# Kernel optimization log

Measured on AMD Instinct MI355X. Metric: run time of the kernel, lower is better.

Reference implementation:

```python
import jax, jax.numpy as jnp
import numpy as np
import math

HIDDEN = 1024
HEADS = 16
HEAD_DIM = HIDDEN // HEADS
TEMP_K = 1000.0  # custom temperature multiplier applied after masking
B, S = 2, 2048


def setup_inputs() -> dict:
    key = jax.random.key(0)
    ks = jax.random.split(key, 4)
    scale = 1.0 / math.sqrt(HIDDEN)
    return {
        "x": jax.random.normal(ks[0], (B, S, HIDDEN), dtype=jnp.float32),
        "W_qkv": jax.random.normal(ks[1], (HIDDEN, 3 * HIDDEN), dtype=jnp.float32) * scale,
        "b_qkv": jnp.zeros((3 * HIDDEN,), dtype=jnp.float32),
        "W_out": jax.random.normal(ks[2], (HIDDEN, HIDDEN), dtype=jnp.float32) * scale,
        "b_out": jnp.zeros((HIDDEN,), dtype=jnp.float32),
    }


def reference(x, W_qkv, b_qkv, W_out, b_out):
    b, s, _ = x.shape
    qkv = x @ W_qkv + b_qkv                                    # [b,s,3*hidden]
    qkv = qkv.reshape(b, s, 3, HEADS, HEAD_DIM)
    qkv = jnp.transpose(qkv, (2, 0, 3, 1, 4))                  # [3,b,h,s,d]
    q, k, v = qkv[0], qkv[1], qkv[2]
    scores = jnp.einsum('bhqd,bhkd->bhqk', q, k) / math.sqrt(HEAD_DIM)
    causal = jnp.tril(jnp.ones((s, s), dtype=bool))            # [s,s]
    scores = jnp.where(causal[None, None], scores, -jnp.inf)
    probs = jax.nn.softmax(scores * TEMP_K, axis=-1)           # temp-scaled softmax
    attn = jnp.einsum('bhqk,bhkd->bhqd', probs, v)             # [b,h,s,d]
    attn = jnp.transpose(attn, (0, 2, 1, 3)).reshape(b, s, HIDDEN)
    return attn @ W_out + b_out
```

## Files before the change

### kernel.cpp

```cpp
#include <hip/hip_runtime.h>
#include <hip/hip_bf16.h>

#define BATCH 2
#define SEQ 2048
#define HID 1024
#define NHEAD 16
#define HDIM 64
#define L2SCALE 180.3368800721f
#define NEGBIG (-1.0e30f)
#define N_ITEMS 512

typedef __bf16 bf16;
typedef __bf16 bf16x4 __attribute__((ext_vector_type(4)));
typedef __bf16 bf16x8 __attribute__((ext_vector_type(8)));
typedef float f32x16 __attribute__((ext_vector_type(16)));

union BQ  { bf16x4 v; unsigned u[2]; };
union BF8 { bf16x8 v; unsigned u[4]; };

__global__ __launch_bounds__(256) void transpose_split_kernel(
    const float* __restrict__ W, bf16* __restrict__ Thi, bf16* __restrict__ Tlo,
    int K, int N)
{
    __shared__ float T[64][65];
    const int tid = threadIdx.x;
    const int kBase = blockIdx.y * 64;
    const int nBase = blockIdx.x * 64;
    {
        const int k0 = tid >> 4;
        const int nc = (tid & 15) * 4;
#pragma unroll
        for (int kk = 0; kk < 4; kk++) {
            int k = k0 + kk * 16;
            float4 v = *(const float4*)(W + (size_t)(kBase + k) * N + nBase + nc);
            T[k][nc] = v.x; T[k][nc + 1] = v.y; T[k][nc + 2] = v.z; T[k][nc + 3] = v.w;
        }
    }
    __syncthreads();
    {
        const int n = tid >> 2;
        const int kc = (tid & 3) * 16;
        bf16x8 h0, h1, l0, l1;
#pragma unroll
        for (int j = 0; j < 8; j++) {
            float a = T[kc + j][n];
            float c = T[kc + 8 + j][n];
            bf16 ha = (bf16)a, hc = (bf16)c;
            h0[j] = ha; h1[j] = hc;
            l0[j] = (bf16)(a - (float)ha);
            l1[j] = (bf16)(c - (float)hc);
        }
        size_t dst = (size_t)(nBase + n) * K + kBase + kc;
        *(bf16x8*)(Thi + dst)     = h0;
        *(bf16x8*)(Thi + dst + 8) = h1;
        if (Tlo) {
            *(bf16x8*)(Tlo + dst)     = l0;
            *(bf16x8*)(Tlo + dst + 8) = l1;
        }
    }
}

__global__ __launch_bounds__(256) void xsplit_kernel(
    const float* __restrict__ X, bf16* __restrict__ Xhi, bf16* __restrict__ Xlo,
    unsigned* __restrict__ ctr)
{
    if (blockIdx.x == 0 && threadIdx.x == 0) *ctr = 0u;
    const int i = blockIdx.x * 256 + threadIdx.x;
    float4 v = ((const float4*)X)[i];
    float xs[4] = {v.x, v.y, v.z, v.w};
    bf16x4 h, l;
#pragma unroll
    for (int j = 0; j < 4; j++) {
        h[j] = (bf16)xs[j];
        l[j] = (bf16)(xs[j] - (float)h[j]);
    }
    ((bf16x4*)Xhi)[i] = h;
    ((bf16x4*)Xlo)[i] = l;
}

__global__ __launch_bounds__(256) void vtrans_kernel(
    const bf16* __restrict__ vv, bf16* __restrict__ vtr)
{
    __shared__ bf16 T[64][72];
    const int tid = threadIdx.x;
    const int bh = blockIdx.y;
    const int st = blockIdx.x;
    const int r  = tid >> 2;
    const int c0 = (tid & 3) * 16;
    const bf16* src = vv + ((size_t)bh * SEQ + st * 64) * HDIM;
    bf16x8 a = *(const bf16x8*)(src + (size_t)r * HDIM + c0);
    bf16x8 b = *(const bf16x8*)(src + (size_t)r * HDIM + c0 + 8);
    *(bf16x8*)&T[r][c0]     = a;
    *(bf16x8*)&T[r][c0 + 8] = b;
    __syncthreads();
    bf16x8 o0, o1;
#pragma unroll
    for (int i = 0; i < 8; i++) {
        o0[i] = T[c0 + i][r];
        o1[i] = T[c0 + 8 + i][r];
    }
    bf16* dst = vtr + ((size_t)bh * HDIM + r) * SEQ + st * 64 + c0;
    *(bf16x8*)(dst)     = o0;
    *(bf16x8*)(dst + 8) = o1;
}

__global__ __launch_bounds__(256) void gemm_qkv_mfma(
    const bf16* __restrict__ Xhi, const bf16* __restrict__ Xlo,
    const bf16* __restrict__ Wthi, const bf16* __restrict__ Wtlo,
    const float* __restrict__ bias,
    bf16* __restrict__ qhi, bf16* __restrict__ qlo,
    bf16* __restrict__ khi, bf16* __restrict__ klo, bf16* __restrict__ vv)
{
    __shared__ __align__(16) bf16 Xh[128][40];
    __shared__ __align__(16) bf16 Xl[128][40];
    __shared__ __align__(16) bf16 Wh[128][40];
    __shared__ __align__(16) bf16 Wl[128][40];

    const int tid = threadIdx.x;
    const int wave = tid >> 6, lane = tid & 63;
    const int lm = lane & 31, lq2 = lane >> 5;
    const int wave_s = wave & 1, wave_n = wave >> 1;
    const int nBase = blockIdx.x * 128;
    const int sBase = blockIdx.y * 128;
    const bool isV = (nBase >= 2 * HID);

    const int sr = tid >> 1, skc = (tid & 1) * 16;

    f32x16 acc[2][2];
#pragma unroll
    for (int st = 0; st < 2; st++)
#pragma unroll
      for (int nt = 0; nt < 2; nt++)
#pragma unroll
        for (int r = 0; r < 16; r++) acc[st][nt][r] = 0.f;

    bf16x8 cx[2], cw[2], cxl[2] = {}, cwl[2] = {};
    {
        size_t xsrc = (size_t)(sBase + sr) * HID + skc;
        size_t wsrc = (size_t)(nBase + sr) * HID + skc;
        cx[0] = *(const bf16x8*)(Xhi + xsrc);
        cx[1] = *(const bf16x8*)(Xhi + xsrc + 8);
        cw[0] = *(const bf16x8*)(Wthi + wsrc);
        cw[1] = *(const bf16x8*)(Wthi + wsrc + 8);
        if (!isV) {
            cxl[0] = *(const bf16x8*)(Xlo + xsrc);
            cxl[1] = *(const bf16x8*)(Xlo + xsrc + 8);
            cwl[0] = *(const bf16x8*)(Wtlo + wsrc);
            cwl[1] = *(const bf16x8*)(Wtlo + wsrc + 8);
        }
    }

    for (int k0 = 0; k0 < HID; k0 += 32) {
        __syncthreads();
        *(bf16x8*)&Xh[sr][skc]     = cx[0];
        *(bf16x8*)&Xh[sr][skc + 8] = cx[1];
        *(bf16x8*)&Wh[sr][skc]     = cw[0];
        *(bf16x8*)&Wh[sr][skc + 8] = cw[1];
        if (!isV) {
            *(bf16x8*)&Xl[sr][skc]     = cxl[0];
            *(bf16x8*)&Xl[sr][skc + 8] = cxl[1];
            *(bf16x8*)&Wl[sr][skc]     = cwl[0];
            *(bf16x8*)&Wl[sr][skc + 8] = cwl[1];
        }
        __syncthreads();

        bf16x8 nx[2] = {}, nw[2] = {}, nxl[2] = {}, nwl[2] = {};
        if (k0 + 32 < HID) {
            size_t xsrc = (size_t)(sBase + sr) * HID + k0 + 32 + skc;
            size_t wsrc = (size_t)(nBase + sr) * HID + k0 + 32 + skc;
            nx[0] = *(const bf16x8*)(Xhi + xsrc);
            nx[1] = *(const bf16x8*)(Xhi + xsrc + 8);
            nw[0] = *(const bf16x8*)(Wthi + wsrc);
            nw[1] = *(const bf16x8*)(Wthi + wsrc + 8);
            if (!isV) {
                nxl[0] = *(const bf16x8*)(Xlo + xsrc);
                nxl[1] = *(const bf16x8*)(Xlo + xsrc + 8);
                nwl[0] = *(const bf16x8*)(Wtlo + wsrc);
                nwl[1] = *(const bf16x8*)(Wtlo + wsrc + 8);
            }
        }

#pragma unroll
        for (int kh = 0; kh < 2; kh++) {
            const int ko = kh * 16 + lq2 * 8;
            bf16x8 aWh[2], aWl[2], bXh[2], bXl[2];
#pragma unroll
            for (int nt = 0; nt < 2; nt++) {
                aWh[nt] = *(bf16x8*)&Wh[wave_n * 64 + nt * 32 + lm][ko];
                if (!isV) aWl[nt] = *(bf16x8*)&Wl[wave_n * 64 + nt * 32 + lm][ko];
            }
#pragma unroll
            for (int st = 0; st < 2; st++) {
                bXh[st] = *(bf16x8*)&Xh[wave_s * 64 + st * 32 + lm][ko];
                if (!isV) bXl[st] = *(bf16x8*)&Xl[wave_s * 64 + st * 32 + lm][ko];
            }
#pragma unroll
            for (int nt = 0; nt < 2; nt++)
#pragma unroll
              for (int st = 0; st < 2; st++) {
                acc[st][nt] = __builtin_amdgcn_mfma_f32_32x32x16_bf16(aWh[nt], bXh[st], acc[st][nt], 0, 0, 0);
                if (!isV) {
                    acc[st][nt] = __builtin_amdgcn_mfma_f32_32x32x16_bf16(aWh[nt], bXl[st], acc[st][nt], 0, 0, 0);
                    acc[st][nt] = __builtin_amdgcn_mfma_f32_32x32x16_bf16(aWl[nt], bXh[st], acc[st][nt], 0, 0, 0);
                }
              }
        }
        cx[0] = nx[0]; cx[1] = nx[1]; cw[0] = nw[0]; cw[1] = nw[1];
        cxl[0] = nxl[0]; cxl[1] = nxl[1]; cwl[0] = nwl[0]; cwl[1] = nwl[1];
    }

#pragma unroll
    for (int st = 0; st < 2; st++) {
        int s = sBase + wave_s * 64 + st * 32 + lm;
        int bb = s >> 11, ss = s & 2047;
#pragma unroll
        for (int nt = 0; nt < 2; nt++) {
#pragma unroll
            for (int q4 = 0; q4 < 4; q4++) {
                int n = nBase + wave_n * 64 + nt * 32 + 8 * q4 + 4 * lq2;
                float4 bv = *(const float4*)(bias + n);
                float vals[4];
                vals[0] = acc[st][nt][q4 * 4 + 0] + bv.x;
                vals[1] = acc[st][nt][q4 * 4 + 1] + bv.y;
                vals[2] = acc[st][nt][q4 * 4 + 2] + bv.z;
                vals[3] = acc[st][nt][q4 * 4 + 3] + bv.w;
                int which = n >> 10, h = (n >> 6) & 15, d = n & 63;
                size_t dst = (((size_t)bb * NHEAD + h) * SEQ + ss) * HDIM + d;
                if (which < 2) {
                    bf16x4 hi4, lo4;
#pragma unroll
                    for (int i = 0; i < 4; i++) {
                        hi4[i] = (bf16)vals[i];
                        lo4[i] = (bf16)(vals[i] - (float)hi4[i]);
                    }
                    bf16* ph = (which == 0) ? qhi : khi;
                    bf16* pl = (which == 0) ? qlo : klo;
                    *(bf16x4*)(ph + dst) = hi4;
                    *(bf16x4*)(pl + dst) = lo4;
                } else {
                    bf16x4 v4;
#pragma unroll
                    for (int i = 0; i < 4; i++) v4[i] = (bf16)vals[i];
                    *(bf16x4*)(vv + dst) = v4;
                }
            }
        }
    }
}

__global__ __launch_bounds__(256) void attn_kernel(
    const bf16* __restrict__ Qhi, const bf16* __restrict__ Qlo,
    const bf16* __restrict__ Khg, const bf16* __restrict__ Klg,
    const bf16* __restrict__ Vtr, bf16* __restrict__ attnbuf,
    unsigned* __restrict__ ctr)
{
    __shared__ __align__(16) bf16 Khs[64][72];
    __shared__ __align__(16) bf16 Kls[64][72];
    __shared__ __align__(16) bf16 Vt [64][72];
    __shared__ int s_item;

    const int tid  = threadIdx.x;
    const int wave = tid >> 6;
    const int lane = tid & 63;
    const int lm   = lane & 31;
    const int lq2  = lane >> 5;

    const int kr  = tid >> 2;
    const int kd0 = (tid & 3) * 16;

    for (;;) {
        if (tid == 0) s_item = (int)atomicAdd(ctr, 1u);
        __syncthreads();
        const int it = s_item;
        if (it >= N_ITEMS) return;
        const int qt = 15 - (it >> 5);
        const int bh = it & 31;
        const int b = bh >> 4, h = bh & 15;
        const size_t headoff = ((size_t)b * NHEAD + h) * SEQ * HDIM;

        const int qg = qt * 128 + wave * 32 + lm;
        bf16x8 qh[4], ql[4];
        {
            const bf16* qph = Qhi + headoff + (size_t)qg * HDIM;
            const bf16* qpl = Qlo + headoff + (size_t)qg * HDIM;
#pragma unroll
            for (int c = 0; c < 4; c++) {
                qh[c] = *(const bf16x8*)(qph + c * 16 + lq2 * 8);
                ql[c] = *(const bf16x8*)(qpl + c * 16 + lq2 * 8);
            }
        }

        f32x16 O0, O1;
#pragma unroll
        for (int r = 0; r < 16; r++) { O0[r] = 0.f; O1[r] = 0.f; }
        float m_run = NEGBIG, l_run = 0.f;

        const int ktmax = 2 * qt + 1;
        bf16x8 kc[4], vc[2];
        {
            size_t kg = headoff + (size_t)kr * HDIM + kd0;
            kc[0] = *(const bf16x8*)(Khg + kg);
            kc[1] = *(const bf16x8*)(Khg + kg + 8);
            kc[2] = *(const bf16x8*)(Klg + kg);
            kc[3] = *(const bf16x8*)(Klg + kg + 8);
            size_t vg = headoff + (size_t)kr * SEQ + kd0;
            vc[0] = *(const bf16x8*)(Vtr + vg);
            vc[1] = *(const bf16x8*)(Vtr + vg + 8);
        }

        for (int kt = 0; kt <= ktmax; kt++) {
            __syncthreads();
            *(bf16x8*)&Khs[kr][kd0]     = kc[0];
            *(bf16x8*)&Khs[kr][kd0 + 8] = kc[1];
            *(bf16x8*)&Kls[kr][kd0]     = kc[2];
            *(bf16x8*)&Kls[kr][kd0 + 8] = kc[3];
            *(bf16x8*)&Vt[kr][kd0]      = vc[0];
            *(bf16x8*)&Vt[kr][kd0 + 8]  = vc[1];
            __syncthreads();

            bf16x8 kn[4], vn[2];
            const bool more = (kt < ktmax);
            if (more) {
                size_t kg = headoff + (size_t)((kt + 1) * 64 + kr) * HDIM + kd0;
                kn[0] = *(const bf16x8*)(Khg + kg);
                kn[1] = *(const bf16x8*)(Khg + kg + 8);
                kn[2] = *(const bf16x8*)(Klg + kg);
                kn[3] = *(const bf16x8*)(Klg + kg + 8);
                size_t vg = headoff + (size_t)kr * SEQ + (kt + 1) * 64 + kd0;
                vn[0] = *(const bf16x8*)(Vtr + vg);
                vn[1] = *(const bf16x8*)(Vtr + vg + 8);
            }

            if (kt * 64 <= qt * 128 + wave * 32 + 31) {
                f32x16 s[2];
#pragma unroll
                for (int r = 0; r < 16; r++) { s[0][r] = 0.f; s[1][r] = 0.f; }
#pragma unroll
                for (int c = 0; c < 4; c++) {
                    bf16x8 ah0 = *(bf16x8*)&Khs[lm][c * 16 + lq2 * 8];
                    bf16x8 al0 = *(bf16x8*)&Kls[lm][c * 16 + lq2 * 8];
                    bf16x8 ah1 = *(bf16x8*)&Khs[32 + lm][c * 16 + lq2 * 8];
                    bf16x8 al1 = *(bf16x8*)&Kls[32 + lm][c * 16 + lq2 * 8];
                    s[0] = __builtin_amdgcn_mfma_f32_32x32x16_bf16(ah0, qh[c], s[0], 0, 0, 0);
                    s[0] = __builtin_amdgcn_mfma_f32_32x32x16_bf16(ah0, ql[c], s[0], 0, 0, 0);
                    s[0] = __builtin_amdgcn_mfma_f32_32x32x16_bf16(al0, qh[c], s[0], 0, 0, 0);
                    s[1] = __builtin_amdgcn_mfma_f32_32x32x16_bf16(ah1, qh[c], s[1], 0, 0, 0);
                    s[1] = __builtin_amdgcn_mfma_f32_32x32x16_bf16(ah1, ql[c], s[1], 0, 0, 0);
                    s[1] = __builtin_amdgcn_mfma_f32_32x32x16_bf16(al1, qh[c], s[1], 0, 0, 0);
                }

                const int kbase = kt * 64 + 4 * lq2;
                const bool needmask = (kt * 64 + 63 > qg);
#pragma unroll
                for (int mt = 0; mt < 2; mt++)
#pragma unroll
                  for (int r = 0; r < 16; r++) {
                    int koff = (r & 3) + 8 * (r >> 2) + 32 * mt;
                    float L = s[mt][r] * L2SCALE;
                    if (needmask && (kbase + koff > qg)) L = NEGBIG;
                    s[mt][r] = L;
                  }

                float vmax = NEGBIG;
#pragma unroll
                for (int r = 0; r < 16; r++)
                    vmax = fmaxf(vmax, fmaxf(s[0][r], s[1][r]));
                vmax = fmaxf(vmax, __shfl_xor(vmax, 32, 64));
                float mnew = fmaxf(m_run, vmax);
                float alpha = exp2f(m_run - mnew);
                float sum = 0.f;
#pragma unroll
                for (int mt = 0; mt < 2; mt++)
#pragma unroll
                  for (int r = 0; r < 16; r++) {
                    s[mt][r] = exp2f(s[mt][r] - mnew);
                    sum += s[mt][r];
                  }
                sum += __shfl_xor(sum, 32, 64);
                l_run = l_run * alpha + sum;
                m_run = mnew;
#pragma unroll
                for (int r = 0; r < 16; r++) { O0[r] *= alpha; O1[r] *= alpha; }

                bf16x8 pfrag[4];
#pragma unroll
                for (int mt = 0; mt < 2; mt++)
#pragma unroll
                  for (int hh = 0; hh < 2; hh++) {
                    BQ A, B;
#pragma unroll
                    for (int i = 0; i < 4; i++) {
                        A.v[i] = (bf16)s[mt][8 * hh + i];
                        B.v[i] = (bf16)s[mt][8 * hh + 4 + i];
                    }
                    unsigned s0_ = lq2 ? A.u[0] : B.u[0];
                    unsigned s1_ = lq2 ? A.u[1] : B.u[1];
                    unsigned r0 = __shfl_xor(s0_, 32, 64);
                    unsigned r1 = __shfl_xor(s1_, 32, 64);
                    BF8 f;
                    f.u[0] = lq2 ? r0 : A.u[0];
                    f.u[1] = lq2 ? r1 : A.u[1];
                    f.u[2] = lq2 ? B.u[0] : r0;
                    f.u[3] = lq2 ? B.u[1] : r1;
                    pfrag[mt * 2 + hh] = f.v;
                  }

#pragma unroll
                for (int c = 0; c < 4; c++) {
                    bf16x8 va0 = *(bf16x8*)&Vt[lm][c * 16 + lq2 * 8];
                    bf16x8 va1 = *(bf16x8*)&Vt[32 + lm][c * 16 + lq2 * 8];
                    O0 = __builtin_amdgcn_mfma_f32_32x32x16_bf16(va0, pfrag[c], O0, 0, 0, 0);
                    O1 = __builtin_amdgcn_mfma_f32_32x32x16_bf16(va1, pfrag[c], O1, 0, 0, 0);
                }
            }

            if (more) {
#pragma unroll
                for (int i = 0; i < 4; i++) kc[i] = kn[i];
                vc[0] = vn[0]; vc[1] = vn[1];
            }
        }

        const float inv = 1.0f / l_run;
        bf16* orow = attnbuf + ((size_t)b * SEQ + qg) * HID + h * HDIM;
#pragma unroll
        for (int g = 0; g < 4; g++) {
            int d0 = 8 * g + 4 * lq2;
            bf16x4 o0, o1;
#pragma unroll
            for (int i = 0; i < 4; i++) {
                o0[i] = (bf16)(O0[4 * g + i] * inv);
                o1[i] = (bf16)(O1[4 * g + i] * inv);
            }
            *(bf16x4*)(orow + d0)      = o0;
            *(bf16x4*)(orow + 32 + d0) = o1;
        }
    }
}

__global__ __launch_bounds__(256) void gemm_out_mfma(
    const bf16* __restrict__ Attn, const bf16* __restrict__ Wt,
    const float* __restrict__ bias, float* __restrict__ out)
{
    __shared__ __align__(16) bf16 Ah[64][40];
    __shared__ __align__(16) bf16 Bh[128][40];

    const int tid = threadIdx.x;
    const int wave = tid >> 6, lane = tid & 63;
    const int lm = lane & 31, lq2 = lane >> 5;
    const int nBase = blockIdx.x * 64;
    const int mBase = blockIdx.y * 128;

    const int sr = tid >> 1, skc = (tid & 1) * 16;
    const int ar = tid >> 2, akc = (tid & 3) * 8;

    f32x16 acc[2];
#pragma unroll
    for (int nt = 0; nt < 2; nt++)
#pragma unroll
      for (int r = 0; r < 16; r++) acc[nt][r] = 0.f;

    bf16x8 cb[2], ca;
    {
        cb[0] = *(const bf16x8*)(Attn + (size_t)(mBase + sr) * HID + skc);
        cb[1] = *(const bf16x8*)(Attn + (size_t)(mBase + sr) * HID + skc + 8);
        ca    = *(const bf16x8*)(Wt + (size_t)(nBase + ar) * HID + akc);
    }

    for (int k0 = 0; k0 < HID; k0 += 32) {
        __syncthreads();
        *(bf16x8*)&Bh[sr][skc]     = cb[0];
        *(bf16x8*)&Bh[sr][skc + 8] = cb[1];
        *(bf16x8*)&Ah[ar][akc]     = ca;
        __syncthreads();

        bf16x8 nb[2] = {}, na = {};
        if (k0 + 32 < HID) {
            nb[0] = *(const bf16x8*)(Attn + (size_t)(mBase + sr) * HID + k0 + 32 + skc);
            nb[1] = *(const bf16x8*)(Attn + (size_t)(mBase + sr) * HID + k0 + 32 + skc + 8);
            na    = *(const bf16x8*)(Wt + (size_t)(nBase + ar) * HID + k0 + 32 + akc);
        }
#pragma unroll
        for (int kh = 0; kh < 2; kh++) {
            const int ko = kh * 16 + lq2 * 8;
            bf16x8 bA  = *(bf16x8*)&Bh[wave * 32 + lm][ko];
            bf16x8 aW0 = *(bf16x8*)&Ah[lm][ko];
            bf16x8 aW1 = *(bf16x8*)&Ah[32 + lm][ko];
            acc[0] = __builtin_amdgcn_mfma_f32_32x32x16_bf16(aW0, bA, acc[0], 0, 0, 0);
            acc[1] = __builtin_amdgcn_mfma_f32_32x32x16_bf16(aW1, bA, acc[1], 0, 0, 0);
        }
        cb[0] = nb[0]; cb[1] = nb[1]; ca = na;
    }

    const int m = mBase + wave * 32 + lm;
#pragma unroll
    for (int nt = 0; nt < 2; nt++) {
#pragma unroll
        for (int q4 = 0; q4 < 4; q4++) {
            int n = nBase + nt * 32 + 8 * q4 + 4 * lq2;
            float4 bv = *(const float4*)(bias + n);
            float4 o;
            o.x = acc[nt][q4 * 4 + 0] + bv.x;
            o.y = acc[nt][q4 * 4 + 1] + bv.y;
            o.z = acc[nt][q4 * 4 + 2] + bv.z;
            o.w = acc[nt][q4 * 4 + 3] + bv.w;
            *(float4*)(out + (size_t)m * HID + n) = o;
        }
    }
}

extern "C" void kernel_launch(void* const* d_in, const int* in_sizes, int n_in,
                              void* d_out, int out_size, void* d_ws, size_t ws_size,
                              hipStream_t stream) {
    const float* x    = (const float*)d_in[0];
    const float* Wqkv = (const float*)d_in[1];
    const float* bqkv = (const float*)d_in[2];
    const float* Wout = (const float*)d_in[3];
    const float* bout = (const float*)d_in[4];
    float* out = (float*)d_out;

    const size_t NW  = (size_t)HID * 3 * HID;
    const size_t NWo = (size_t)HID * HID;
    const size_t NT  = (size_t)BATCH * NHEAD * SEQ * HDIM;
    bf16* Wthi = (bf16*)d_ws;
    bf16* Wtlo = Wthi + NW;
    bf16* Wot  = Wtlo + NW;
    bf16* qhi  = Wot + NWo;
    bf16* qlo  = qhi + NT;
    bf16* khi  = qlo + NT;
    bf16* klo  = khi + NT;
    bf16* vv   = klo + NT;
    bf16* attnbuf = vv + NT;
    bf16* Xhi  = attnbuf;
    bf16* Xlo  = attnbuf + NT;
    bf16* vtr  = Xlo;
    unsigned* ctr = (unsigned*)(Xlo + NT);

    xsplit_kernel<<<dim3((BATCH * SEQ * HID) / 1024), 256, 0, stream>>>(x, Xhi, Xlo, ctr);
    transpose_split_kernel<<<dim3(3 * HID / 64, HID / 64), 256, 0, stream>>>(
        Wqkv, Wthi, Wtlo, HID, 3 * HID);
    transpose_split_kernel<<<dim3(HID / 64, HID / 64), 256, 0, stream>>>(
        Wout, Wot, nullptr, HID, HID);
    gemm_qkv_mfma<<<dim3(3 * HID / 128, BATCH * SEQ / 128), 256, 0, stream>>>(
        Xhi, Xlo, Wthi, Wtlo, bqkv, qhi, qlo, khi, klo, vv);
    vtrans_kernel<<<dim3(SEQ / 64, BATCH * NHEAD), 256, 0, stream>>>(vv, vtr);
    attn_kernel<<<dim3(1024), 256, 0, stream>>>(
        qhi, qlo, khi, klo, vtr, attnbuf, ctr);
    gemm_out_mfma<<<dim3(HID / 64, BATCH * SEQ / 128), 256, 0, stream>>>(
        attnbuf, Wot, bout, out);
}
```

Before: 277.4 us.

## Replace atomic work queue with static split-KV schedule plus combine kernel

Drops the atomic-counter persistent scheduler for attention. A static table of 30 slots per head gives each block a balanced chunk of at most 12 key tiles, and long query tiles are split across 2–3 blocks. Partial outputs and their (m,l) statistics go to scratch buffers reused from dead workspace, and a new combine kernel merges them. Masking is also limited to the diagonal tiles. This evens out causal load across the 960 blocks, at the cost of an extra launch, partial-output traffic, and rounding the partials to bf16.

```diff
diff --git a/kernel.cpp b/kernel.cpp
--- a/kernel.cpp
+++ b/kernel.cpp
@@ -8,7 +8,6 @@
 #define HDIM 64
 #define L2SCALE 180.3368800721f
 #define NEGBIG (-1.0e30f)
-#define N_ITEMS 512
 
 typedef __bf16 bf16;
 typedef __bf16 bf16x4 __attribute__((ext_vector_type(4)));
@@ -17,6 +16,11 @@
 
 union BQ  { bf16x4 v; unsigned u[2]; };
 union BF8 { bf16x8 v; unsigned u[4]; };
+
+__device__ __constant__ int TAB_QT[30]  = {5,6,7,8,9,10,11,11,12,12,13,13,14,14,15,15, 4,10, 3,9,15, 2,8,14, 1,7,13, 0,6,12};
+__device__ __constant__ int TAB_K0[30]  = {0,0,0,0,0,0,0,12,0,12,0,12,0,12,0,12, 0,12, 0,12,24, 0,12,24, 0,12,24, 0,12,24};
+__device__ __constant__ int TAB_NIT[30] = {12,12,12,12,12,12,12,12,12,12,12,12,12,12,12,12, 10,10, 8,8,8, 6,6,6, 4,4,4, 2,2,2};
+__device__ __constant__ int TAB_PID[30] = {-1,0,2,4,6,8,10,11,12,13,15,16,18,19,21,22, -1,9, -1,7,23, -1,5,20, -1,3,17, -1,1,14};
 
 __global__ __launch_bounds__(256) void transpose_split_kernel(
     const float* __restrict__ W, bf16* __restrict__ Thi, bf16* __restrict__ Tlo,
@@ -61,10 +65,8 @@
 }
 
 __global__ __launch_bounds__(256) void xsplit_kernel(
-    const float* __restrict__ X, bf16* __restrict__ Xhi, bf16* __restrict__ Xlo,
-    unsigned* __restrict__ ctr)
+    const float* __restrict__ X, bf16* __restrict__ Xhi, bf16* __restrict__ Xlo)
 {
-    if (blockIdx.x == 0 && threadIdx.x == 0) *ctr = 0u;
     const int i = blockIdx.x * 256 + threadIdx.x;
     float4 v = ((const float4*)X)[i];
     float xs[4] = {v.x, v.y, v.z, v.w};
@@ -252,12 +254,11 @@
     const bf16* __restrict__ Qhi, const bf16* __restrict__ Qlo,
     const bf16* __restrict__ Khg, const bf16* __restrict__ Klg,
     const bf16* __restrict__ Vtr, bf16* __restrict__ attnbuf,
-    unsigned* __restrict__ ctr)
+    bf16* __restrict__ PartO, float* __restrict__ Mls)
 {
     __shared__ __align__(16) bf16 Khs[64][72];
     __shared__ __align__(16) bf16 Kls[64][72];
     __shared__ __align__(16) bf16 Vt [64][72];
-    __shared__ int s_item;
 
     const int tid  = threadIdx.x;
     const int wave = tid >> 6;
@@ -268,159 +269,168 @@
     const int kr  = tid >> 2;
     const int kd0 = (tid & 3) * 16;
 
-    for (;;) {
-        if (tid == 0) s_item = (int)atomicAdd(ctr, 1u);
+    const int slot = blockIdx.x >> 5;
+    const int bh   = blockIdx.x & 31;
+    const int qt   = TAB_QT[slot];
+    const int kt0  = TAB_K0[slot];
+    const int nit  = TAB_NIT[slot];
+    const int pid  = TAB_PID[slot];
+    const int b = bh >> 4, h = bh & 15;
+    const size_t headoff = ((size_t)b * NHEAD + h) * SEQ * HDIM;
+
+    const int ql_loc = wave * 32 + lm;
+    const int qg = qt * 128 + ql_loc;
+    bf16x8 qh[4], qlr[4];
+    {
+        const bf16* qph = Qhi + headoff + (size_t)qg * HDIM;
+        const bf16* qpl = Qlo + headoff + (size_t)qg * HDIM;
+#pragma unroll
+        for (int c = 0; c < 4; c++) {
+            qh[c]  = *(const bf16x8*)(qph + c * 16 + lq2 * 8);
+            qlr[c] = *(const bf16x8*)(qpl + c * 16 + lq2 * 8);
+        }
+    }
+
+    f32x16 O0, O1;
+#pragma unroll
+    for (int r = 0; r < 16; r++) { O0[r] = 0.f; O1[r] = 0.f; }
+    float m_run = NEGBIG, l_run = 0.f;
+
+    const int wave_qmin = qt * 128 + wave * 32;
+    const int ktend = kt0 + nit;
+
+    bf16x8 kc[4], vc[2];
+    {
+        size_t kg = headoff + (size_t)(kt0 * 64 + kr) * HDIM + kd0;
+        kc[0] = *(const bf16x8*)(Khg + kg);
+        kc[1] = *(const bf16x8*)(Khg + kg + 8);
+        kc[2] = *(const bf16x8*)(Klg + kg);
+        kc[3] = *(const bf16x8*)(Klg + kg + 8);
+        size_t vg = headoff + (size_t)kr * SEQ + kt0 * 64 + kd0;
+        vc[0] = *(const bf16x8*)(Vtr + vg);
+        vc[1] = *(const bf16x8*)(Vtr + vg + 8);
+    }
+
+    for (int kt = kt0; kt < ktend; kt++) {
         __syncthreads();
-        const int it = s_item;
-        if (it >= N_ITEMS) return;
-        const int qt = 15 - (it >> 5);
-        const int bh = it & 31;
-        const int b = bh >> 4, h = bh & 15;
-        const size_t headoff = ((size_t)b * NHEAD + h) * SEQ * HDIM;
-
-        const int qg = qt * 128 + wave * 32 + lm;
-        bf16x8 qh[4], ql[4];
-        {
-            const bf16* qph = Qhi + headoff + (size_t)qg * HDIM;
-            const bf16* qpl = Qlo + headoff + (size_t)qg * HDIM;
+        *(bf16x8*)&Khs[kr][kd0]     = kc[0];
+        *(bf16x8*)&Khs[kr][kd0 + 8] = kc[1];
+        *(bf16x8*)&Kls[kr][kd0]     = kc[2];
+        *(bf16x8*)&Kls[kr][kd0 + 8] = kc[3];
+        *(bf16x8*)&Vt[kr][kd0]      = vc[0];
+        *(bf16x8*)&Vt[kr][kd0 + 8]  = vc[1];
+        __syncthreads();
+
+        bf16x8 kn[4], vn[2];
+        const bool more = (kt + 1 < ktend);
+        if (more) {
+            size_t kg = headoff + (size_t)((kt + 1) * 64 + kr) * HDIM + kd0;
+            kn[0] = *(const bf16x8*)(Khg + kg);
+            kn[1] = *(const bf16x8*)(Khg + kg + 8);
+            kn[2] = *(const bf16x8*)(Klg + kg);
+            kn[3] = *(const bf16x8*)(Klg + kg + 8);
+            size_t vg = headoff + (size_t)kr * SEQ + (kt + 1) * 64 + kd0;
+            vn[0] = *(const bf16x8*)(Vtr + vg);
+            vn[1] = *(const bf16x8*)(Vtr + vg + 8);
+        }
+
+        if (kt * 64 <= wave_qmin + 31) {
+            f32x16 s[2];
+#pragma unroll
+            for (int r = 0; r < 16; r++) { s[0][r] = 0.f; s[1][r] = 0.f; }
 #pragma unroll
             for (int c = 0; c < 4; c++) {
-                qh[c] = *(const bf16x8*)(qph + c * 16 + lq2 * 8);
-                ql[c] = *(const bf16x8*)(qpl + c * 16 + lq2 * 8);
-            }
-        }
-
-        f32x16 O0, O1;
-#pragma unroll
-        for (int r = 0; r < 16; r++) { O0[r] = 0.f; O1[r] = 0.f; }
-        float m_run = NEGBIG, l_run = 0.f;
-
-        const int ktmax = 2 * qt + 1;
-        bf16x8 kc[4], vc[2];
-        {
-            size_t kg = headoff + (size_t)kr * HDIM + kd0;
-            kc[0] = *(const bf16x8*)(Khg + kg);
-            kc[1] = *(const bf16x8*)(Khg + kg + 8);
-            kc[2] = *(const bf16x8*)(Klg + kg);
-            kc[3] = *(const bf16x8*)(Klg + kg + 8);
-            size_t vg = headoff + (size_t)kr * SEQ + kd0;
-            vc[0] = *(const bf16x8*)(Vtr + vg);
-            vc[1] = *(const bf16x8*)(Vtr + vg + 8);
-        }
-
-        for (int kt = 0; kt <= ktmax; kt++) {
-            __syncthreads();
-            *(bf16x8*)&Khs[kr][kd0]     = kc[0];
-            *(bf16x8*)&Khs[kr][kd0 + 8] = kc[1];
-            *(bf16x8*)&Kls[kr][kd0]     = kc[2];
-            *(bf16x8*)&Kls[kr][kd0 + 8] = kc[3];
-            *(bf16x8*)&Vt[kr][kd0]      = vc[0];
-            *(bf16x8*)&Vt[kr][kd0 + 8]  = vc[1];
-            __syncthreads();
-
-            bf16x8 kn[4], vn[2];
-            const bool more = (kt < ktmax);
-            if (more) {
-                size_t kg = headoff + (size_t)((kt + 1) * 64 + kr) * HDIM + kd0;
-                kn[0] = *(const bf16x8*)(Khg + kg);
-                kn[1] = *(const bf16x8*)(Khg + kg + 8);
-                kn[2] = *(const bf16x8*)(Klg + kg);
-                kn[3] = *(const bf16x8*)(Klg + kg + 8);
-                size_t vg = headoff + (size_t)kr * SEQ + (kt + 1) * 64 + kd0;
-                vn[0] = *(const bf16x8*)(Vtr + vg);
-                vn[1] = *(const bf16x8*)(Vtr + vg + 8);
-            }
-
-            if (kt * 64 <= qt * 128 + wave * 32 + 31) {
-                f32x16 s[2];
-#pragma unroll
-                for (int r = 0; r < 16; r++) { s[0][r] = 0.f; s[1][r] = 0.f; }
-#pragma unroll
-                for (int c = 0; c < 4; c++) {
-                    bf16x8 ah0 = *(bf16x8*)&Khs[lm][c * 16 + lq2 * 8];
-                    bf16x8 al0 = *(bf16x8*)&Kls[lm][c * 16 + lq2 * 8];
-                    bf16x8 ah1 = *(bf16x8*)&Khs[32 + lm][c * 16 + lq2 * 8];
-                    bf16x8 al1 = *(bf16x8*)&Kls[32 + lm][c * 16 + lq2 * 8];
-                    s[0] = __builtin_amdgcn_mfma_f32_32x32x16_bf16(ah0, qh[c], s[0], 0, 0, 0);
-                    s[0] = __builtin_amdgcn_mfma_f32_32x32x16_bf16(ah0, ql[c], s[0], 0, 0, 0);
-                    s[0] = __builtin_amdgcn_mfma_f32_32x32x16_bf16(al0, qh[c], s[0], 0, 0, 0);
-                    s[1] = __builtin_amdgcn_mfma_f32_32x32x16_bf16(ah1, qh[c], s[1], 0, 0, 0);
-                    s[1] = __builtin_amdgcn_mfma_f32_32x32x16_bf16(ah1, ql[c], s[1], 0, 0, 0);
-                    s[1] = __builtin_amdgcn_mfma_f32_32x32x16_bf16(al1, qh[c], s[1], 0, 0, 0);
-                }
-
+                bf16x8 ah0 = *(bf16x8*)&Khs[lm][c * 16 + lq2 * 8];
+                bf16x8 al0 = *(bf16x8*)&Kls[lm][c * 16 + lq2 * 8];
+                bf16x8 ah1 = *(bf16x8*)&Khs[32 + lm][c * 16 + lq2 * 8];
+                bf16x8 al1 = *(bf16x8*)&Kls[32 + lm][c * 16 + lq2 * 8];
+                s[0] = __builtin_amdgcn_mfma_f32_32x32x16_bf16(ah0, qh[c],  s[0], 0, 0, 0);
+                s[0] = __builtin_amdgcn_mfma_f32_32x32x16_bf16(ah0, qlr[c], s[0], 0, 0, 0);
+                s[0] = __builtin_amdgcn_mfma_f32_32x32x16_bf16(al0, qh[c],  s[0], 0, 0, 0);
+                s[1] = __builtin_amdgcn_mfma_f32_32x32x16_bf16(ah1, qh[c],  s[1], 0, 0, 0);
+                s[1] = __builtin_amdgcn_mfma_f32_32x32x16_bf16(ah1, qlr[c], s[1], 0, 0, 0);
+                s[1] = __builtin_amdgcn_mfma_f32_32x32x16_bf16(al1, qh[c],  s[1], 0, 0, 0);
+            }
+
+            if (kt * 64 + 63 > wave_qmin) {
                 const int kbase = kt * 64 + 4 * lq2;
-                const bool needmask = (kt * 64 + 63 > qg);
 #pragma unroll
                 for (int mt = 0; mt < 2; mt++)
 #pragma unroll
                   for (int r = 0; r < 16; r++) {
                     int koff = (r & 3) + 8 * (r >> 2) + 32 * mt;
                     float L = s[mt][r] * L2SCALE;
-                    if (needmask && (kbase + koff > qg)) L = NEGBIG;
+                    if (kbase + koff > qg) L = NEGBIG;
                     s[mt][r] = L;
                   }
-
-                float vmax = NEGBIG;
-#pragma unroll
-                for (int r = 0; r < 16; r++)
-                    vmax = fmaxf(vmax, fmaxf(s[0][r], s[1][r]));
-                vmax = fmaxf(vmax, __shfl_xor(vmax, 32, 64));
-                float mnew = fmaxf(m_run, vmax);
-                float alpha = exp2f(m_run - mnew);
-                float sum = 0.f;
+            } else {
 #pragma unroll
                 for (int mt = 0; mt < 2; mt++)
 #pragma unroll
-                  for (int r = 0; r < 16; r++) {
-                    s[mt][r] = exp2f(s[mt][r] - mnew);
-                    sum += s[mt][r];
-                  }
-                sum += __shfl_xor(sum, 32, 64);
-                l_run = l_run * alpha + sum;
-                m_run = mnew;
-#pragma unroll
-                for (int r = 0; r < 16; r++) { O0[r] *= alpha; O1[r] *= alpha; }
-
-                bf16x8 pfrag[4];
-#pragma unroll
-                for (int mt = 0; mt < 2; mt++)
-#pragma unroll
-                  for (int hh = 0; hh < 2; hh++) {
-                    BQ A, B;
-#pragma unroll
-                    for (int i = 0; i < 4; i++) {
-                        A.v[i] = (bf16)s[mt][8 * hh + i];
-                        B.v[i] = (bf16)s[mt][8 * hh + 4 + i];
-                    }
-                    unsigned s0_ = lq2 ? A.u[0] : B.u[0];
-                    unsigned s1_ = lq2 ? A.u[1] : B.u[1];
-                    unsigned r0 = __shfl_xor(s0_, 32, 64);
-                    unsigned r1 = __shfl_xor(s1_, 32, 64);
-                    BF8 f;
-                    f.u[0] = lq2 ? r0 : A.u[0];
-                    f.u[1] = lq2 ? r1 : A.u[1];
-                    f.u[2] = lq2 ? B.u[0] : r0;
-                    f.u[3] = lq2 ? B.u[1] : r1;
-                    pfrag[mt * 2 + hh] = f.v;
-                  }
-
-#pragma unroll
-                for (int c = 0; c < 4; c++) {
-                    bf16x8 va0 = *(bf16x8*)&Vt[lm][c * 16 + lq2 * 8];
-                    bf16x8 va1 = *(bf16x8*)&Vt[32 + lm][c * 16 + lq2 * 8];
-                    O0 = __builtin_amdgcn_mfma_f32_32x32x16_bf16(va0, pfrag[c], O0, 0, 0, 0);
-                    O1 = __builtin_amdgcn_mfma_f32_32x32x16_bf16(va1, pfrag[c], O1, 0, 0, 0);
+                  for (int r = 0; r < 16; r++) s[mt][r] *= L2SCALE;
+            }
+
+            float vmax = NEGBIG;
+#pragma unroll
+            for (int r = 0; r < 16; r++)
+                vmax = fmaxf(vmax, fmaxf(s[0][r], s[1][r]));
+            vmax = fmaxf(vmax, __shfl_xor(vmax, 32, 64));
+            float mnew = fmaxf(m_run, vmax);
+            float alpha = exp2f(m_run - mnew);
+            float sum = 0.f;
+#pragma unroll
+            for (int mt = 0; mt < 2; mt++)
+#pragma unroll
+              for (int r = 0; r < 16; r++) {
+                s[mt][r] = exp2f(s[mt][r] - mnew);
+                sum += s[mt][r];
+              }
+            sum += __shfl_xor(sum, 32, 64);
+            l_run = l_run * alpha + sum;
+            m_run = mnew;
+#pragma unroll
+            for (int r = 0; r < 16; r++) { O0[r] *= alpha; O1[r] *= alpha; }
+
+            bf16x8 pfrag[4];
+#pragma unroll
+            for (int mt = 0; mt < 2; mt++)
+#pragma unroll
+              for (int hh = 0; hh < 2; hh++) {
+                BQ A, B;
+#pragma unroll
+                for (int i = 0; i < 4; i++) {
+                    A.v[i] = (bf16)s[mt][8 * hh + i];
+                    B.v[i] = (bf16)s[mt][8 * hh + 4 + i];
                 }
-            }
-
-            if (more) {
-#pragma unroll
-                for (int i = 0; i < 4; i++) kc[i] = kn[i];
-                vc[0] = vn[0]; vc[1] = vn[1];
-            }
-        }
-
+                unsigned s0_ = lq2 ? A.u[0] : B.u[0];
+                unsigned s1_ = lq2 ? A.u[1] : B.u[1];
+                unsigned r0 = __shfl_xor(s0_, 32, 64);
+                unsigned r1 = __shfl_xor(s1_, 32, 64);
+                BF8 f;
+                f.u[0] = lq2 ? r0 : A.u[0];
+                f.u[1] = lq2 ? r1 : A.u[1];
+                f.u[2] = lq2 ? B.u[0] : r0;
+                f.u[3] = lq2 ? B.u[1] : r1;
+                pfrag[mt * 2 + hh] = f.v;
+              }
+
+#pragma unroll
+            for (int c = 0; c < 4; c++) {
+                bf16x8 va0 = *(bf16x8*)&Vt[lm][c * 16 + lq2 * 8];
+                bf16x8 va1 = *(bf16x8*)&Vt[32 + lm][c * 16 + lq2 * 8];
+                O0 = __builtin_amdgcn_mfma_f32_32x32x16_bf16(va0, pfrag[c], O0, 0, 0, 0);
+                O1 = __builtin_amdgcn_mfma_f32_32x32x16_bf16(va1, pfrag[c], O1, 0, 0, 0);
+            }
+        }
+
+        if (more) {
+#pragma unroll
+            for (int i = 0; i < 4; i++) kc[i] = kn[i];
+            vc[0] = vn[0]; vc[1] = vn[1];
+        }
+    }
+
+    if (pid < 0) {
         const float inv = 1.0f / l_run;
         bf16* orow = attnbuf + ((size_t)b * SEQ + qg) * HID + h * HDIM;
 #pragma unroll
@@ -435,6 +445,78 @@
             *(bf16x4*)(orow + d0)      = o0;
             *(bf16x4*)(orow + 32 + d0) = o1;
         }
+    } else {
+        bf16* prow = PartO + (((size_t)pid * 32 + bh) * 128 + ql_loc) * HDIM;
+#pragma unroll
+        for (int g = 0; g < 4; g++) {
+            int d0 = 8 * g + 4 * lq2;
+            bf16x4 o0, o1;
+#pragma unroll
+            for (int i = 0; i < 4; i++) {
+                o0[i] = (bf16)O0[4 * g + i];
+                o1[i] = (bf16)O1[4 * g + i];
+            }
+            *(bf16x4*)(prow + d0)      = o0;
+            *(bf16x4*)(prow + 32 + d0) = o1;
+        }
+        if (lq2 == 0) {
+            float2 ml = make_float2(m_run, l_run);
+            *(float2*)&Mls[(((size_t)pid * 32 + bh) * 128 + ql_loc) * 2] = ml;
+        }
+    }
+}
+
+__global__ __launch_bounds__(256) void attn_combine(
+    const bf16* __restrict__ PartO, const float* __restrict__ Mls,
+    bf16* __restrict__ attnbuf)
+{
+    const int tid = threadIdx.x;
+    const int qt = 6 + blockIdx.x / 32;
+    const int bh = blockIdx.x & 31;
+    const int b = bh >> 4, h = bh & 15;
+    const int qrow = tid >> 1;
+    const int dh = (tid & 1) * 32;
+
+    int pid0, nch;
+    if (qt < 12) { pid0 = 2 * (qt - 6); nch = 2; }
+    else         { pid0 = 12 + 3 * (qt - 12); nch = 3; }
+
+    float mv[3], lv[3];
+    float M = NEGBIG;
+#pragma unroll
+    for (int c = 0; c < 3; c++) {
+        if (c < nch) {
+            float2 ml = *(const float2*)&Mls[(((size_t)(pid0 + c) * 32 + bh) * 128 + qrow) * 2];
+            mv[c] = ml.x; lv[c] = ml.y;
+            M = fmaxf(M, mv[c]);
+        }
+    }
+    float L = 0.f;
+    float acc[32];
+#pragma unroll
+    for (int i = 0; i < 32; i++) acc[i] = 0.f;
+#pragma unroll
+    for (int c = 0; c < 3; c++) {
+        if (c < nch) {
+            float w = exp2f(mv[c] - M);
+            L += w * lv[c];
+            const bf16* p = PartO + (((size_t)(pid0 + c) * 32 + bh) * 128 + qrow) * HDIM + dh;
+#pragma unroll
+            for (int g = 0; g < 4; g++) {
+                bf16x8 v = *(const bf16x8*)(p + g * 8);
+#pragma unroll
+                for (int i = 0; i < 8; i++) acc[g * 8 + i] += w * (float)v[i];
+            }
+        }
+    }
+    const float inv = 1.0f / L;
+    bf16* orow = attnbuf + ((size_t)b * SEQ + qt * 128 + qrow) * HID + h * HDIM + dh;
+#pragma unroll
+    for (int g = 0; g < 4; g++) {
+        bf16x8 o;
+#pragma unroll
+        for (int i = 0; i < 8; i++) o[i] = (bf16)(acc[g * 8 + i] * inv);
+        *(bf16x8*)(orow + g * 8) = o;
     }
 }
 
@@ -534,9 +616,10 @@
     bf16* Xhi  = attnbuf;
     bf16* Xlo  = attnbuf + NT;
     bf16* vtr  = Xlo;
-    unsigned* ctr = (unsigned*)(Xlo + NT);
-
-    xsplit_kernel<<<dim3((BATCH * SEQ * HID) / 1024), 256, 0, stream>>>(x, Xhi, Xlo, ctr);
+    bf16* PartO = Wthi;
+    float* Mls  = (float*)vv;
+
+    xsplit_kernel<<<dim3((BATCH * SEQ * HID) / 1024), 256, 0, stream>>>(x, Xhi, Xlo);
     transpose_split_kernel<<<dim3(3 * HID / 64, HID / 64), 256, 0, stream>>>(
         Wqkv, Wthi, Wtlo, HID, 3 * HID);
     transpose_split_kernel<<<dim3(HID / 64, HID / 64), 256, 0, stream>>>(
@@ -544,8 +627,9 @@
     gemm_qkv_mfma<<<dim3(3 * HID / 128, BATCH * SEQ / 128), 256, 0, stream>>>(
         Xhi, Xlo, Wthi, Wtlo, bqkv, qhi, qlo, khi, klo, vv);
     vtrans_kernel<<<dim3(SEQ / 64, BATCH * NHEAD), 256, 0, stream>>>(vv, vtr);
-    attn_kernel<<<dim3(1024), 256, 0, stream>>>(
-        qhi, qlo, khi, klo, vtr, attnbuf, ctr);
+    attn_kernel<<<dim3(960), 256, 0, stream>>>(
+        qhi, qlo, khi, klo, vtr, attnbuf, PartO, Mls);
+    attn_combine<<<dim3(320), 256, 0, stream>>>(PartO, Mls, attnbuf);
     gemm_out_mfma<<<dim3(HID / 64, BATCH * SEQ / 128), 256, 0, stream>>>(
         attnbuf, Wot, bout, out);
 }
```

After: 254.3 us. -8.3%, faster.
